# Kernel optimization log

Measured on AMD Instinct MI355X. Metric: run time of the kernel, lower is better.

The kernel has to match this reference:

```python
import jax, jax.numpy as jnp
import numpy as np

B, S, D = 2, 2048, 2048
H, KVH = 32, 8
HD = D // H            # 64
N_REP = H // KVH       # 4
THETA = 10000.0


def _rope_tables(seq_len, half_dim):
    inv = 1.0 / (THETA ** (np.arange(0, half_dim, dtype=np.float32) * 2.0 / (2 * half_dim)))
    t = np.arange(seq_len, dtype=np.float32)
    f = np.outer(t, inv)  # (S, half_dim)
    return jnp.asarray(np.cos(f)), jnp.asarray(np.sin(f))


def setup_inputs() -> dict:
    key = jax.random.key(0)
    ks = jax.random.split(key, 5)
    sc = 0.02
    x = jax.random.normal(ks[0], (B, S, D), dtype=jnp.float32)
    W_q = jax.random.normal(ks[1], (D, H * HD), dtype=jnp.float32) * sc
    W_k = jax.random.normal(ks[2], (D, KVH * HD), dtype=jnp.float32) * sc
    W_v = jax.random.normal(ks[3], (D, KVH * HD), dtype=jnp.float32) * sc
    W_o = jax.random.normal(ks[4], (D, D), dtype=jnp.float32) * sc
    b_o = jnp.zeros((D,), dtype=jnp.float32)
    freqs_cos, freqs_sin = _rope_tables(S, HD // 2)
    return {"x": x, "W_q": W_q, "W_k": W_k, "W_v": W_v, "W_o": W_o,
            "b_o": b_o, "freqs_cos": freqs_cos, "freqs_sin": freqs_sin}


def _apply_rope(t, cos, sin):
    # t: (B, S, h, HD); cos/sin: (S, HD//2), broadcast over batch/heads
    t1, t2 = t[..., 0::2], t[..., 1::2]
    c = cos[None, :, None, :]
    s = sin[None, :, None, :]
    r1 = t1 * c - t2 * s
    r2 = t1 * s + t2 * c
    # interleave back to (..., HD)
    return jnp.stack([r1, r2], axis=-1).reshape(t.shape)


def reference(x, W_q, W_k, W_v, W_o, b_o, freqs_cos, freqs_sin):
    b, s, _ = x.shape
    Q = (x @ W_q).reshape(b, s, H, HD)
    K = (x @ W_k).reshape(b, s, KVH, HD)
    V = (x @ W_v).reshape(b, s, KVH, HD)
    Q = _apply_rope(Q, freqs_cos, freqs_sin)
    K = _apply_rope(K, freqs_cos, freqs_sin)
    # GQA: repeat KV heads (matches torch repeat_interleave along head dim)
    K = jnp.repeat(K, N_REP, axis=2)  # (b, s, H, HD)
    V = jnp.repeat(V, N_REP, axis=2)
    scores = jnp.einsum('bqhd,bkhd->bhqk', Q, K) / jnp.sqrt(jnp.float32(HD))
    causal = jnp.triu(jnp.ones((s, s), dtype=bool), k=1)
    scores = jnp.where(causal[None, None, :, :], -jnp.inf, scores)
    attn = jax.nn.softmax(scores, axis=-1)  # dropout=0 / eval mode -> identity
    ctx = jnp.einsum('bhqk,bkhd->bqhd', attn, V).reshape(b, s, D)
    return ctx @ W_o + b_o
```

## Files before the change

kernel.cpp:

```cpp
#include <hip/hip_runtime.h>
#include <hip/hip_bf16.h>

#define BB 2
#define SS 2048
#define DD 2048
#define HH 32
#define KVH 8
#define HD 64
#define QKV_LD 3072

typedef unsigned short u16;
typedef unsigned int u32;
typedef __attribute__((ext_vector_type(8))) short s16x8;
typedef __attribute__((ext_vector_type(4))) float f32x4;
typedef __attribute__((ext_vector_type(4))) u16 u16x4;
typedef __attribute__((ext_vector_type(2))) u32 u32x2;
typedef __attribute__((ext_vector_type(4))) u32 u32x4;

#define MFMA(a, b, c) __builtin_amdgcn_mfma_f32_16x16x32_bf16((a), (b), (c), 0, 0, 0)

__device__ __forceinline__ u16 f2bf(float f) {
  union { float f; u32 u; } x; x.f = f;
  u32 r = x.u + 0x7fffu + ((x.u >> 16) & 1u);
  return (u16)(r >> 16);
}
__device__ __forceinline__ float bf2f(u32 u) {
  union { u32 u; float f; } x; x.u = u << 16;
  return x.f;
}
__device__ __forceinline__ u32 cvtpk(float a, float b) {
  u32 r;
  asm("v_cvt_pk_bf16_f32 %0, %1, %2" : "=v"(r) : "v"(a), "v"(b));
  return r;
}

__device__ __forceinline__ void gload16(const void* g, void* l) {
  __builtin_amdgcn_global_load_lds((const __attribute__((address_space(1))) unsigned int*)g,
                                   (__attribute__((address_space(3))) unsigned int*)l, 16, 0, 0);
}

__device__ __forceinline__ s16x8 lds_frag(const u16* base, int row, int c) {
  return *(const s16x8*)(base + (row << 6) + (((c ^ (row & 7)) << 3)));
}

__global__ void tcast(const float* __restrict__ src, int scols, u16* __restrict__ dst, int dld) {
  __shared__ float tt[32][33];
  int c0 = blockIdx.x << 5, r0 = blockIdx.y << 5;
  int tx = threadIdx.x, ty = threadIdx.y;
#pragma unroll
  for (int j = 0; j < 4; ++j)
    tt[ty + j * 8][tx] = src[(size_t)(r0 + ty + j * 8) * scols + c0 + tx];
  __syncthreads();
#pragma unroll
  for (int j = 0; j < 4; ++j)
    dst[(size_t)(c0 + ty + j * 8) * dld + r0 + tx] = f2bf(tt[tx][ty + j * 8]);
}

__global__ void rope_k(u16* __restrict__ qkv, const float* __restrict__ fc, const float* __restrict__ fs) {
  const float SCLQ = 0.125f * 1.44269504f;
  int idx = blockIdx.x * 256 + threadIdx.x;
  int row = idx / 320;
  int p4 = (idx - row * 320) << 2;
  int s = row & (SS - 1);
  int col, i;
  float sc;
  if (p4 < 1024) { col = p4 << 1; i = p4 & 31; sc = SCLQ; }
  else { int pk = p4 - 1024; col = 2048 + (pk << 1); i = pk & 31; sc = 1.0f; }
  size_t base = (size_t)row * QKV_LD + col;
  u32x4 v = *(const u32x4*)(qkv + base);
  const float4 c4 = *(const float4*)(fc + s * 32 + i);
  const float4 s4 = *(const float4*)(fs + s * 32 + i);
  float cc[4] = {c4.x, c4.y, c4.z, c4.w};
  float ss[4] = {s4.x, s4.y, s4.z, s4.w};
  u32x4 o;
#pragma unroll
  for (int j = 0; j < 4; ++j) {
    float t1 = bf2f(v[j] & 0xffffu), t2 = bf2f(v[j] >> 16);
    float r1 = (t1 * cc[j] - t2 * ss[j]) * sc;
    float r2 = (t1 * ss[j] + t2 * cc[j]) * sc;
    o[j] = cvtpk(r1, r2);
  }
  *(u32x4*)(qkv + base) = o;
}

__global__ void transpose_v(const u16* __restrict__ qkv, u16* __restrict__ vt) {
  __shared__ u16 tt[32][33];
  int c0 = blockIdx.x << 5, r0 = blockIdx.y << 5;
  int tx = threadIdx.x, ty = threadIdx.y;
#pragma unroll
  for (int j = 0; j < 4; ++j)
    tt[ty + j * 8][tx] = qkv[(size_t)(r0 + ty + j * 8) * QKV_LD + 2560 + c0 + tx];
  __syncthreads();
#pragma unroll
  for (int j = 0; j < 4; ++j) {
    int c = c0 + ty + j * 8;
    int rr = r0 + tx;
    int b = rr >> 11, s = rr & (SS - 1), g = c >> 6, d = c & 63;
    vt[(size_t)((((b << 3) + g) << 6) + d) * SS + s] = tt[tx][ty + j * 8];
  }
}

template<bool AF32, bool SWZ>
__global__ __launch_bounds__(512) void gemm_bt(const u16* __restrict__ A, const float* __restrict__ Af,
                                               const u16* __restrict__ BT,
                                               int K, u16* __restrict__ Cb, float* __restrict__ Cf,
                                               const float* __restrict__ bias, int ldc) {
  __shared__ alignas(16) u16 lds[2 * 128 * 64];
  u16* Al = lds;
  u16* Bl = lds + 128 * 64;
  const int t = threadIdx.x, w = t >> 6, lane = t & 63;
  const int q_l = lane & 15, gh = lane >> 4;
  int m0, n0;
  if constexpr (SWZ) {
    const int gx = gridDim.x, nxy = gx * gridDim.y;
    int xy = blockIdx.y * gx + blockIdx.x;
    xy = (xy & 7) * (nxy >> 3) + (xy >> 3);
    n0 = (xy % gx) << 7;
    m0 = (xy / gx) << 7;
  } else {
    m0 = blockIdx.y << 7;
    n0 = blockIdx.x << 7;
  }
  const int wm = (w >> 2) << 6;
  const int wn = (w & 3) << 5;
  f32x4 acc[4][2] = {};

  for (int k0 = 0; k0 < K; k0 += 64) {
#pragma unroll
    for (int i = 0; i < 2; ++i) {
      int o = (i << 13) + (t << 4);
      int row = o >> 7;
      int sblk = ((o >> 4) & 7) ^ (row & 7);
      int cs = sblk << 4;
      if constexpr (AF32) {
        const float* ap = Af + (size_t)(m0 + row) * K + k0 + (sblk << 3);
        float4 a0 = *(const float4*)ap;
        float4 a1 = *(const float4*)(ap + 4);
        u32x4 pk;
        pk[0] = cvtpk(a0.x, a0.y);
        pk[1] = cvtpk(a0.z, a0.w);
        pk[2] = cvtpk(a1.x, a1.y);
        pk[3] = cvtpk(a1.z, a1.w);
        *(u32x4*)((char*)Al + o) = pk;
      } else {
        gload16((const char*)A + (((size_t)(m0 + row) * K + k0) << 1) + cs, (char*)Al + o);
      }
      gload16((const char*)BT + (((size_t)(n0 + row) * K + k0) << 1) + cs, (char*)Bl + o);
    }
    __syncthreads();
#pragma unroll
    for (int kk = 0; kk < 64; kk += 32) {
      const int c = (kk >> 3) + gh;
      s16x8 af[4], bfr[2];
#pragma unroll
      for (int mi = 0; mi < 4; ++mi) af[mi] = lds_frag(Al, wm + (mi << 4) + q_l, c);
#pragma unroll
      for (int ni = 0; ni < 2; ++ni) bfr[ni] = lds_frag(Bl, wn + (ni << 4) + q_l, c);
#pragma unroll
      for (int mi = 0; mi < 4; ++mi)
#pragma unroll
        for (int ni = 0; ni < 2; ++ni)
          acc[mi][ni] = MFMA(af[mi], bfr[ni], acc[mi][ni]);
    }
    __syncthreads();
  }

  const int rbase = m0 + wm + (gh << 2);
  const int cbase = n0 + wn + q_l;
  if (Cf != nullptr) {
#pragma unroll
    for (int mi = 0; mi < 4; ++mi)
#pragma unroll
      for (int ni = 0; ni < 2; ++ni) {
        int col = cbase + (ni << 4);
        float bv = bias[col];
#pragma unroll
        for (int r = 0; r < 4; ++r)
          Cf[(size_t)(rbase + (mi << 4) + r) * ldc + col] = acc[mi][ni][r] + bv;
      }
  } else {
#pragma unroll
    for (int mi = 0; mi < 4; ++mi)
#pragma unroll
      for (int ni = 0; ni < 2; ++ni) {
        int col = cbase + (ni << 4);
#pragma unroll
        for (int r = 0; r < 4; ++r)
          Cb[(size_t)(rbase + (mi << 4) + r) * ldc + col] = f2bf(acc[mi][ni][r]);
      }
  }
}

__global__ __launch_bounds__(256, 4) void attn_k(const u16* __restrict__ qkv, const u16* __restrict__ vt,
                                                 u16* __restrict__ ctx) {
  __shared__ alignas(16) u16 sK[2][64 * 64];
  __shared__ alignas(16) u16 sV[2][64 * 64];
  __shared__ alignas(16) u16 sP[4][16 * 64];
  const int bid = blockIdx.x;
  const int qt = 31 - (bid >> 6);
  const int h = bid & 31, b = (bid >> 5) & 1;
  const int q0 = qt << 6, g = h >> 2;
  const int t = threadIdx.x, w = t >> 6, lane = t & 63;
  const int q_l = lane & 15, gh = lane >> 4;

  const s16x8 ones = { (short)0x3F80, (short)0x3F80, (short)0x3F80, (short)0x3F80,
                       (short)0x3F80, (short)0x3F80, (short)0x3F80, (short)0x3F80 };

  const int srow = (w << 3) + (lane >> 3);
  const int blk = lane & 7;
  const int lw0 = (srow << 6) + ((blk ^ (lane >> 3)) << 3);
  const u16* kg = qkv + (size_t)((b << 11) + srow) * QKV_LD + 2048 + (g << 6) + (blk << 3);
  const u16* vg = vt + (size_t)((((b << 3) + g) << 6) + srow) * SS + (blk << 3);

  const int qrow = (b << 11) + q0 + (w << 4) + q_l;
  const u16* qptr = qkv + (size_t)qrow * QKV_LD + (h << 6) + (gh << 3);
  s16x8 qa0 = *(const s16x8*)qptr;
  s16x8 qa1 = *(const s16x8*)(qptr + 32);

  f32x4 o[4] = {};
  f32x4 lacc = {};
  float m1 = -INFINITY;
  const int myq = q0 + (w << 4) + q_l;

  s16x8 kr[2], vr[2];
#pragma unroll
  for (int i = 0; i < 2; ++i) {
    kr[i] = *(const s16x8*)(kg + (size_t)(i << 5) * QKV_LD);
    vr[i] = *(const s16x8*)(vg + (size_t)(i << 5) * SS);
  }
#pragma unroll
  for (int i = 0; i < 2; ++i) {
    *(s16x8*)(sK[0] + lw0 + (i << 11)) = kr[i];
    *(s16x8*)(sV[0] + lw0 + (i << 11)) = vr[i];
  }
  __syncthreads();

  for (int kt_i = 0; kt_i <= qt; ++kt_i) {
    const int k0 = kt_i << 6;
    const int cur = kt_i & 1;
    const u16* Kl = sK[cur];
    const u16* Vl = sV[cur];
    if (kt_i < qt) {
      const int kn = k0 + 64;
#pragma unroll
      for (int i = 0; i < 2; ++i) {
        kr[i] = *(const s16x8*)(kg + (size_t)(kn + (i << 5)) * QKV_LD);
        vr[i] = *(const s16x8*)(vg + (size_t)(i << 5) * SS + kn);
      }
    }

    f32x4 sacc[4];
    __builtin_amdgcn_s_setprio(1);
#pragma unroll
    for (int nc = 0; nc < 4; ++nc) {
      f32x4 a = {};
      a = MFMA(lds_frag(Kl, (nc << 4) + q_l, gh), qa0, a);
      a = MFMA(lds_frag(Kl, (nc << 4) + q_l, 4 + gh), qa1, a);
      sacc[nc] = a;
    }
    __builtin_amdgcn_s_setprio(0);

    float pv[4][4];
    if (kt_i == qt) {
#pragma unroll
      for (int nc = 0; nc < 4; ++nc) {
        int kb = k0 + (nc << 4) + (gh << 2);
#pragma unroll
        for (int r = 0; r < 4; ++r) {
          float v = sacc[nc][r];
          if (kb + r > myq) v = -INFINITY;
          pv[nc][r] = v;
        }
      }
    } else {
#pragma unroll
      for (int nc = 0; nc < 4; ++nc)
#pragma unroll
        for (int r = 0; r < 4; ++r)
          pv[nc][r] = sacc[nc][r];
    }

    float ta = fmaxf(fmaxf(pv[0][0], pv[0][1]), pv[0][2]);
    float tb = fmaxf(fmaxf(pv[0][3], pv[1][0]), pv[1][1]);
    float tc = fmaxf(fmaxf(pv[1][2], pv[1][3]), pv[2][0]);
    float td = fmaxf(fmaxf(pv[2][1], pv[2][2]), pv[2][3]);
    float te = fmaxf(fmaxf(pv[3][0], pv[3][1]), pv[3][2]);
    float tmax = fmaxf(fmaxf(fmaxf(ta, tb), fmaxf(tc, td)), fmaxf(te, pv[3][3]));
    if (__any(tmax > m1 + 8.f)) {
      float rmax = tmax;
      rmax = fmaxf(rmax, __shfl_xor(rmax, 16));
      rmax = fmaxf(rmax, __shfl_xor(rmax, 32));
      float mn = fmaxf(m1, rmax);
      float alpha = exp2f(m1 - mn);
      m1 = mn;
#pragma unroll
      for (int r = 0; r < 4; ++r) lacc[r] *= alpha;
#pragma unroll
      for (int dc = 0; dc < 4; ++dc)
#pragma unroll
        for (int r = 0; r < 4; ++r) o[dc][r] *= alpha;
    }

#pragma unroll
    for (int nc = 0; nc < 4; ++nc)
#pragma unroll
      for (int r = 0; r < 4; ++r)
        pv[nc][r] = exp2f(pv[nc][r] - m1);

    u16* pb = sP[w];
#pragma unroll
    for (int nc = 0; nc < 4; ++nc) {
      u32x2 pw;
      pw[0] = cvtpk(pv[nc][0], pv[nc][1]);
      pw[1] = cvtpk(pv[nc][2], pv[nc][3]);
      int byte = (q_l << 7) + (((((nc << 1) + (gh >> 1)) ^ (q_l & 7)) << 4)) + ((gh & 1) << 3);
      *(u32x2*)((char*)pb + byte) = pw;
    }
    asm volatile("s_waitcnt lgkmcnt(0)" ::: "memory");
    __builtin_amdgcn_sched_barrier(0);

    s16x8 pa0 = lds_frag(pb, q_l, gh);
    s16x8 pa1 = lds_frag(pb, q_l, 4 + gh);
    __builtin_amdgcn_s_setprio(1);
#pragma unroll
    for (int dc = 0; dc < 4; ++dc) {
      o[dc] = MFMA(lds_frag(Vl, (dc << 4) + q_l, gh), pa0, o[dc]);
      o[dc] = MFMA(lds_frag(Vl, (dc << 4) + q_l, 4 + gh), pa1, o[dc]);
    }
    lacc = MFMA(ones, pa0, lacc);
    lacc = MFMA(ones, pa1, lacc);
    __builtin_amdgcn_s_setprio(0);

    if (kt_i < qt) {
#pragma unroll
      for (int i = 0; i < 2; ++i) {
        *(s16x8*)(sK[cur ^ 1] + lw0 + (i << 11)) = kr[i];
        *(s16x8*)(sV[cur ^ 1] + lw0 + (i << 11)) = vr[i];
      }
    }
    __syncthreads();
  }

  float inv = 1.0f / lacc[0];
  u16* crow = ctx + (size_t)((b << 11) + myq) * DD + (h << 6) + (gh << 2);
#pragma unroll
  for (int dc = 0; dc < 4; ++dc) {
    u32x2 ov;
    ov[0] = cvtpk(o[dc][0] * inv, o[dc][1] * inv);
    ov[1] = cvtpk(o[dc][2] * inv, o[dc][3] * inv);
    *(u32x2*)(crow + (dc << 4)) = ov;
  }
}

extern "C" void kernel_launch(void* const* d_in, const int* in_sizes, int n_in,
                              void* d_out, int out_size, void* d_ws, size_t ws_size,
                              hipStream_t stream) {
  const float* x  = (const float*)d_in[0];
  const float* Wq = (const float*)d_in[1];
  const float* Wk = (const float*)d_in[2];
  const float* Wv = (const float*)d_in[3];
  const float* Wo = (const float*)d_in[4];
  const float* bo = (const float*)d_in[5];
  const float* fc = (const float*)d_in[6];
  const float* fs = (const float*)d_in[7];
  float* out = (float*)d_out;

  u16* ws   = (u16*)d_ws;
  u16* ctx  = ws;
  u16* wT   = ctx + 8388608;
  u16* qkv  = wT + 6291456;
  u16* vt   = qkv + 12582912;
  u16* woT  = wT;

  dim3 b32(32, 8, 1);

  tcast<<<dim3(64, 64), b32, 0, stream>>>(Wq, 2048, wT, 2048);
  tcast<<<dim3(16, 64), b32, 0, stream>>>(Wk, 512, wT + (size_t)2048 * 2048, 2048);
  tcast<<<dim3(16, 64), b32, 0, stream>>>(Wv, 512, wT + (size_t)2560 * 2048, 2048);

  gemm_bt<true, true><<<dim3(24, 32), 512, 0, stream>>>(nullptr, x, wT, 2048, qkv, nullptr, nullptr, QKV_LD);

  tcast<<<dim3(64, 64), b32, 0, stream>>>(Wo, 2048, woT, 2048);

  rope_k<<<5120, 256, 0, stream>>>(qkv, fc, fs);
  transpose_v<<<dim3(16, 128), b32, 0, stream>>>(qkv, vt);

  attn_k<<<2048, 256, 0, stream>>>(qkv, vt, ctx);

  gemm_bt<false, false><<<dim3(16, 32), 512, 0, stream>>>(ctx, nullptr, woT, 2048, nullptr, out, bo, 2048);
}
```

Before: 208.6 us.

## Stage fp32 A tiles in LDS via async loads and convert at fragment read

For the fp32-input GEMM path, the A tile is no longer loaded into registers, converted to bf16 and stored to LDS. It is now brought into LDS as fp32 with async global_load_lds, and the bf16 conversion happens when each MFMA fragment is read. LDS use grows by half for that variant, and launch bounds now request two blocks per CU. This removes the register round-trip and the load-use stall, but fp32 fragments double LDS read traffic and move conversion work into the inner loop.

```diff
diff --git a/kernel.cpp b/kernel.cpp
--- a/kernel.cpp
+++ b/kernel.cpp
@@ -41,6 +41,18 @@
 
 __device__ __forceinline__ s16x8 lds_frag(const u16* base, int row, int c) {
   return *(const s16x8*)(base + (row << 6) + (((c ^ (row & 7)) << 3)));
+}
+
+__device__ __forceinline__ s16x8 lds_frag_f32(const float* base, int row, int c) {
+  const char* p = (const char*)base + (row << 8) + ((c ^ (row & 7)) << 5);
+  f32x4 lo = *(const f32x4*)p;
+  f32x4 hi = *(const f32x4*)(p + 16);
+  union { u32x4 u; s16x8 s; } r;
+  r.u[0] = cvtpk(lo[0], lo[1]);
+  r.u[1] = cvtpk(lo[2], lo[3]);
+  r.u[2] = cvtpk(hi[0], hi[1]);
+  r.u[3] = cvtpk(hi[2], hi[3]);
+  return r.s;
 }
 
 __global__ void tcast(const float* __restrict__ src, int scols, u16* __restrict__ dst, int dld) {
@@ -101,13 +113,14 @@
 }
 
 template<bool AF32, bool SWZ>
-__global__ __launch_bounds__(512) void gemm_bt(const u16* __restrict__ A, const float* __restrict__ Af,
-                                               const u16* __restrict__ BT,
-                                               int K, u16* __restrict__ Cb, float* __restrict__ Cf,
-                                               const float* __restrict__ bias, int ldc) {
-  __shared__ alignas(16) u16 lds[2 * 128 * 64];
-  u16* Al = lds;
-  u16* Bl = lds + 128 * 64;
+__global__ __launch_bounds__(512, 2) void gemm_bt(const u16* __restrict__ A, const float* __restrict__ Af,
+                                                  const u16* __restrict__ BT,
+                                                  int K, u16* __restrict__ Cb, float* __restrict__ Cf,
+                                                  const float* __restrict__ bias, int ldc) {
+  __shared__ alignas(16) u16 lds[AF32 ? 3 * 128 * 64 : 2 * 128 * 64];
+  u16* Bl = lds;
+  u16* Al = lds + 128 * 64;
+  float* AlF = (float*)(lds + 128 * 64);
   const int t = threadIdx.x, w = t >> 6, lane = t & 63;
   const int q_l = lane & 15, gh = lane >> 4;
   int m0, n0;
@@ -131,29 +144,37 @@
       int o = (i << 13) + (t << 4);
       int row = o >> 7;
       int sblk = ((o >> 4) & 7) ^ (row & 7);
-      int cs = sblk << 4;
-      if constexpr (AF32) {
-        const float* ap = Af + (size_t)(m0 + row) * K + k0 + (sblk << 3);
-        float4 a0 = *(const float4*)ap;
-        float4 a1 = *(const float4*)(ap + 4);
-        u32x4 pk;
-        pk[0] = cvtpk(a0.x, a0.y);
-        pk[1] = cvtpk(a0.z, a0.w);
-        pk[2] = cvtpk(a1.x, a1.y);
-        pk[3] = cvtpk(a1.z, a1.w);
-        *(u32x4*)((char*)Al + o) = pk;
-      } else {
-        gload16((const char*)A + (((size_t)(m0 + row) * K + k0) << 1) + cs, (char*)Al + o);
-      }
-      gload16((const char*)BT + (((size_t)(n0 + row) * K + k0) << 1) + cs, (char*)Bl + o);
+      gload16((const char*)BT + (((size_t)(n0 + row) * K + k0) << 1) + (sblk << 4), (char*)Bl + o);
+    }
+    if constexpr (AF32) {
+#pragma unroll
+      for (int j = 0; j < 4; ++j) {
+        int b = (j << 13) + (t << 4);
+        int row = b >> 8;
+        int gsrc = ((b >> 5) & 7) ^ (row & 7);
+        int half = (b >> 4) & 1;
+        gload16(Af + (size_t)(m0 + row) * K + k0 + (gsrc << 3) + (half << 2), (char*)AlF + b);
+      }
+    } else {
+#pragma unroll
+      for (int i = 0; i < 2; ++i) {
+        int o = (i << 13) + (t << 4);
+        int row = o >> 7;
+        int sblk = ((o >> 4) & 7) ^ (row & 7);
+        gload16((const char*)A + (((size_t)(m0 + row) * K + k0) << 1) + (sblk << 4), (char*)Al + o);
+      }
     }
     __syncthreads();
+
 #pragma unroll
     for (int kk = 0; kk < 64; kk += 32) {
       const int c = (kk >> 3) + gh;
       s16x8 af[4], bfr[2];
 #pragma unroll
-      for (int mi = 0; mi < 4; ++mi) af[mi] = lds_frag(Al, wm + (mi << 4) + q_l, c);
+      for (int mi = 0; mi < 4; ++mi) {
+        if constexpr (AF32) af[mi] = lds_frag_f32(AlF, wm + (mi << 4) + q_l, c);
+        else af[mi] = lds_frag(Al, wm + (mi << 4) + q_l, c);
+      }
 #pragma unroll
       for (int ni = 0; ni < 2; ++ni) bfr[ni] = lds_frag(Bl, wn + (ni << 4) + q_l, c);
 #pragma unroll
```

Result: slower. 222.2 us (+6.5%).
